# Kernel tuning notes

Measured on AMD Instinct MI355X. Metric: run time of the kernel, lower is better.

Reference implementation:

```python
import jax, jax.numpy as jnp
import numpy as np

B, IN, OUT = 32768, 1024, 1024

def setup_inputs() -> dict:
    key = jax.random.key(0)
    k1, k2, k3 = jax.random.split(key, 3)
    bound = float(np.sqrt(6.0 / (IN + OUT)))  # xavier_uniform gain=1
    x = jax.random.normal(k1, (B, IN), dtype=jnp.float32)
    weight = jax.random.uniform(k2, (OUT, IN), dtype=jnp.float32, minval=-bound, maxval=bound)
    gate = jnp.abs(jax.random.uniform(k3, (OUT, IN), dtype=jnp.float32, minval=-bound, maxval=bound))  # one_sided init
    bias = jnp.zeros((OUT,), dtype=jnp.float32)
    return {"x": x, "weight": weight, "gate": gate, "bias": bias}

def reference(x, weight, gate, bias):
    # in_bin = sign
    layer_in = jnp.sign(x)
    # drop_weights: weight * binarize_gate(gate) where binarize_gate = (sign(gate)+1)/2
    gate_mask = (jnp.sign(gate) + 1.0) * 0.5
    w = weight * gate_mask
    # weight_bin = sign (gated-off entries stay 0 since sign(0)=0)
    w = jnp.sign(w)
    # F.linear: x @ w.T + bias
    layer_out = jnp.einsum('bi,oi->bo', layer_in, w) + bias
    # adaptive scaling: abs-mean of raw input per row, abs-mean of raw weight per output
    in_scale = jnp.mean(jnp.abs(x), axis=1, keepdims=True)       # [B,1]
    weight_scale = jnp.mean(jnp.abs(weight), axis=1)             # [OUT]
    return in_scale * weight_scale * layer_out
```

## Files before the change

### kernel.cpp

```cpp
#include <hip/hip_runtime.h>

#define B_DIM 32768
#define IN_DIM 1024
#define OUT_DIM 1024

typedef int v4i __attribute__((ext_vector_type(4)));
typedef int v16i __attribute__((ext_vector_type(16)));

__device__ __forceinline__ int sgnb(float v) {
    return (v > 0.f) ? 1 : ((v < 0.f) ? 0xff : 0);
}
__device__ __forceinline__ int gsgnb(float w, float g) {
    return (g < 0.f) ? 0 : sgnb(w);
}

__global__ __launch_bounds__(256) void prep_kernel(
    const float* __restrict__ x, const float* __restrict__ w,
    const float* __restrict__ g,
    signed char* __restrict__ sx, signed char* __restrict__ wb,
    float* __restrict__ xscale, float* __restrict__ wscale) {
    const int wave = threadIdx.x >> 6;
    const int lane = threadIdx.x & 63;
    const int bq = blockIdx.x;
    if (bq < B_DIM / 4) {
        const int row = bq * 4 + wave;
        const float4* xr = (const float4*)(x + (size_t)row * IN_DIM);
        int* sr = (int*)(sx + (size_t)row * IN_DIM);
        float asum = 0.f;
#pragma unroll
        for (int it = 0; it < 4; ++it) {
            float4 v = xr[it * 64 + lane];
            asum += fabsf(v.x) + fabsf(v.y) + fabsf(v.z) + fabsf(v.w);
            sr[it * 64 + lane] =
                sgnb(v.x) | (sgnb(v.y) << 8) | (sgnb(v.z) << 16) | (sgnb(v.w) << 24);
        }
#pragma unroll
        for (int off = 32; off >= 1; off >>= 1) asum += __shfl_xor(asum, off, 64);
        if (lane == 0) xscale[row] = asum * (1.0f / IN_DIM);
    } else {
        const int row = (bq - B_DIM / 4) * 4 + wave;
        const float4* wr = (const float4*)(w + (size_t)row * IN_DIM);
        const float4* gr = (const float4*)(g + (size_t)row * IN_DIM);
        int* sr = (int*)(wb + (size_t)row * IN_DIM);
        float asum = 0.f;
#pragma unroll
        for (int it = 0; it < 4; ++it) {
            float4 wv = wr[it * 64 + lane];
            float4 gv = gr[it * 64 + lane];
            asum += fabsf(wv.x) + fabsf(wv.y) + fabsf(wv.z) + fabsf(wv.w);
            sr[it * 64 + lane] = gsgnb(wv.x, gv.x) | (gsgnb(wv.y, gv.y) << 8) |
                                 (gsgnb(wv.z, gv.z) << 16) | (gsgnb(wv.w, gv.w) << 24);
        }
#pragma unroll
        for (int off = 32; off >= 1; off >>= 1) asum += __shfl_xor(asum, off, 64);
        if (lane == 0) wscale[row] = asum * (1.0f / IN_DIM);
    }
}

__global__ __launch_bounds__(512, 2) void gemm_i8_kernel(
    const signed char* __restrict__ A,
    const signed char* __restrict__ Bw,
    const float* __restrict__ xscale,
    const float* __restrict__ wscale,
    const float* __restrict__ bias,
    float* __restrict__ out) {
    __shared__ signed char smA[2][16384];
    __shared__ signed char smB[2][16384];

    const int t = threadIdx.x;
    const int wave = t >> 6, lane = t & 63;
    const int swz = (blockIdx.x & 7) * 64 + (blockIdx.x >> 3);
    const int bm = swz >> 2;
    const int bn = swz & 3;
    const int wr = wave >> 2, wc = wave & 3;
    const int r32 = lane & 31;
    const int kh_eff = ((lane >> 5) << 4) ^ (((lane >> 2) & 1) << 4);

    int aoff[4], boff[2];
#pragma unroll
    for (int m = 0; m < 4; ++m) aoff[m] = (wr * 128 + m * 32 + r32) * 32 + kh_eff;
#pragma unroll
    for (int n = 0; n < 2; ++n) boff[n] = (wc * 64 + n * 32 + r32) * 32 + kh_eff;

    const int soff = wave * 1024 + lane * 16;
    const int s_row = soff >> 5;
    const int s_kh = (soff & 16) ^ (((s_row >> 2) & 1) << 4);
    const size_t arow0 = (size_t)bm * 256;
    const size_t brow0 = (size_t)bn * 256;
    const signed char* aSrc = A + (((size_t)(arow0 + s_row)) << 10) + s_kh;
    const signed char* bSrc = Bw + (((size_t)(brow0 + s_row)) << 10) + s_kh;

    v16i acc[4][2];
#pragma unroll
    for (int m = 0; m < 4; ++m)
#pragma unroll
        for (int n = 0; n < 2; ++n)
#pragma unroll
            for (int j = 0; j < 16; ++j) acc[m][n][j] = 0;

#define ISSUE_A(P, KS, K0)                                                      \
    __builtin_amdgcn_global_load_lds(                                           \
        (const __attribute__((address_space(1))) void*)(aSrc + (K0) + (KS)*32), \
        (__attribute__((address_space(3))) void*)(&smA[P][(KS)*8192] + wave * 1024), \
        16, 0, 0)
#define ISSUE_B(P, KS, K0)                                                      \
    __builtin_amdgcn_global_load_lds(                                           \
        (const __attribute__((address_space(1))) void*)(bSrc + (K0) + (KS)*32), \
        (__attribute__((address_space(3))) void*)(&smB[P][(KS)*8192] + wave * 1024), \
        16, 0, 0)

#define PHASE(P, KS, DOPREF, K0N, VMASM)                                        \
    {                                                                           \
        v4i af[4], bf[2];                                                       \
        _Pragma("unroll") for (int m = 0; m < 4; ++m)                           \
            af[m] = *(const v4i*)(&smA[P][(KS)*8192] + aoff[m]);                \
        _Pragma("unroll") for (int n = 0; n < 2; ++n)                           \
            bf[n] = *(const v4i*)(&smB[P][(KS)*8192] + boff[n]);                \
        if (DOPREF) {                                                           \
            ISSUE_A((P) ^ 1, KS, K0N);                                          \
            ISSUE_B((P) ^ 1, KS, K0N);                                          \
        }                                                                       \
        __builtin_amdgcn_s_barrier();                                           \
        __builtin_amdgcn_s_setprio(1);                                          \
        _Pragma("unroll") for (int m = 0; m < 4; ++m) {                         \
            acc[m][0] = __builtin_amdgcn_mfma_i32_32x32x32_i8(af[m], bf[0],     \
                                                              acc[m][0], 0, 0, 0); \
            acc[m][1] = __builtin_amdgcn_mfma_i32_32x32x32_i8(af[m], bf[1],     \
                                                              acc[m][1], 0, 0, 0); \
        }                                                                       \
        __builtin_amdgcn_s_setprio(0);                                          \
        VMASM;                                                                  \
        __builtin_amdgcn_s_barrier();                                           \
    }

    ISSUE_A(0, 0, 0);
    ISSUE_B(0, 0, 0);
    ISSUE_A(0, 1, 0);
    ISSUE_B(0, 1, 0);
    asm volatile("s_waitcnt vmcnt(2)" ::: "memory");
    __builtin_amdgcn_s_barrier();

#pragma unroll 1
    for (int kt = 0; kt < 14; kt += 2) {
        PHASE(0, 0, 1, (kt + 1) * 64, asm volatile("s_waitcnt vmcnt(2)" ::: "memory"));
        PHASE(0, 1, 1, (kt + 1) * 64, asm volatile("s_waitcnt vmcnt(2)" ::: "memory"));
        PHASE(1, 0, 1, (kt + 2) * 64, asm volatile("s_waitcnt vmcnt(2)" ::: "memory"));
        PHASE(1, 1, 1, (kt + 2) * 64, asm volatile("s_waitcnt vmcnt(2)" ::: "memory"));
    }
    PHASE(0, 0, 1, 15 * 64, asm volatile("s_waitcnt vmcnt(2)" ::: "memory"));
    PHASE(0, 1, 1, 15 * 64, asm volatile("s_waitcnt vmcnt(2)" ::: "memory"));
    PHASE(1, 0, 0, 0, asm volatile("s_waitcnt vmcnt(0)" ::: "memory"));
    PHASE(1, 1, 0, 0, (void)0);

#undef PHASE
#undef ISSUE_A
#undef ISSUE_B

    const int col = lane & 31;
    const int rb = 4 * (lane >> 5);
    float wsc[2], bv[2];
    int gcolv[2];
#pragma unroll
    for (int n = 0; n < 2; ++n) {
        gcolv[n] = bn * 256 + wc * 64 + n * 32 + col;
        wsc[n] = wscale[gcolv[n]];
        bv[n] = bias[gcolv[n]];
    }
#pragma unroll
    for (int m = 0; m < 4; ++m) {
#pragma unroll
        for (int j = 0; j < 16; ++j) {
            const int grow = bm * 256 + wr * 128 + m * 32 + (j & 3) + 8 * (j >> 2) + rb;
            const float is = xscale[grow];
#pragma unroll
            for (int n = 0; n < 2; ++n) {
                out[(size_t)grow * OUT_DIM + gcolv[n]] =
                    is * wsc[n] * ((float)acc[m][n][j] + bv[n]);
            }
        }
    }
}

extern "C" void kernel_launch(void* const* d_in, const int* in_sizes, int n_in,
                              void* d_out, int out_size, void* d_ws, size_t ws_size,
                              hipStream_t stream) {
    const float* x = (const float*)d_in[0];
    const float* w = (const float*)d_in[1];
    const float* g = (const float*)d_in[2];
    const float* bias = (const float*)d_in[3];
    float* out = (float*)d_out;

    signed char* sx = (signed char*)d_ws;
    signed char* wb = sx + (size_t)B_DIM * IN_DIM;
    float* xscale = (float*)(wb + (size_t)OUT_DIM * IN_DIM);
    float* wscale = xscale + B_DIM;

    prep_kernel<<<B_DIM / 4 + OUT_DIM / 4, 256, 0, stream>>>(x, w, g, sx, wb,
                                                             xscale, wscale);
    gemm_i8_kernel<<<(B_DIM / 256) * (OUT_DIM / 256), 512, 0, stream>>>(
        sx, wb, xscale, wscale, bias, out);
}
```

Measured before the change: 288.3 us.

## Deepen int8 GEMM LDS pipeline to four stages with 64-byte K tiles

```diff
diff --git a/kernel.cpp b/kernel.cpp
--- a/kernel.cpp
+++ b/kernel.cpp
@@ -64,8 +64,8 @@
     const float* __restrict__ wscale,
     const float* __restrict__ bias,
     float* __restrict__ out) {
-    __shared__ signed char smA[2][16384];
-    __shared__ signed char smB[2][16384];
+    __shared__ signed char smA[4][16384];
+    __shared__ signed char smB[4][16384];
 
     const int t = threadIdx.x;
     const int wave = t >> 6, lane = t & 63;
@@ -74,21 +74,20 @@
     const int bn = swz & 3;
     const int wr = wave >> 2, wc = wave & 3;
     const int r32 = lane & 31;
-    const int kh_eff = ((lane >> 5) << 4) ^ (((lane >> 2) & 1) << 4);
+    const int kh = (lane >> 5) << 4;
+    const int fsw = ((r32 >> 1) & 3) << 4;
+    const int c0 = kh ^ fsw;
 
     int aoff[4], boff[2];
 #pragma unroll
-    for (int m = 0; m < 4; ++m) aoff[m] = (wr * 128 + m * 32 + r32) * 32 + kh_eff;
-#pragma unroll
-    for (int n = 0; n < 2; ++n) boff[n] = (wc * 64 + n * 32 + r32) * 32 + kh_eff;
-
-    const int soff = wave * 1024 + lane * 16;
-    const int s_row = soff >> 5;
-    const int s_kh = (soff & 16) ^ (((s_row >> 2) & 1) << 4);
-    const size_t arow0 = (size_t)bm * 256;
-    const size_t brow0 = (size_t)bn * 256;
-    const signed char* aSrc = A + (((size_t)(arow0 + s_row)) << 10) + s_kh;
-    const signed char* bSrc = Bw + (((size_t)(brow0 + s_row)) << 10) + s_kh;
+    for (int m = 0; m < 4; ++m) aoff[m] = (wr * 128 + m * 32 + r32) * 64 + c0;
+#pragma unroll
+    for (int n = 0; n < 2; ++n) boff[n] = (wc * 64 + n * 32 + r32) * 64 + c0;
+
+    const int sc = (((t & 3) ^ ((t >> 3) & 3)) << 4);
+    const signed char* aS = A + ((size_t)(bm * 256 + (t >> 2)) << 10) + sc;
+    const signed char* bS = Bw + ((size_t)(bn * 256 + (t >> 2)) << 10) + sc;
+    const int ldsW = wave * 1024;
 
     v16i acc[4][2];
 #pragma unroll
@@ -98,28 +97,29 @@
 #pragma unroll
             for (int j = 0; j < 16; ++j) acc[m][n][j] = 0;
 
-#define ISSUE_A(P, KS, K0)                                                      \
+#define GLDS(SRC, DST)                                                          \
     __builtin_amdgcn_global_load_lds(                                           \
-        (const __attribute__((address_space(1))) void*)(aSrc + (K0) + (KS)*32), \
-        (__attribute__((address_space(3))) void*)(&smA[P][(KS)*8192] + wave * 1024), \
-        16, 0, 0)
-#define ISSUE_B(P, KS, K0)                                                      \
-    __builtin_amdgcn_global_load_lds(                                           \
-        (const __attribute__((address_space(1))) void*)(bSrc + (K0) + (KS)*32), \
-        (__attribute__((address_space(3))) void*)(&smB[P][(KS)*8192] + wave * 1024), \
-        16, 0, 0)
-
-#define PHASE(P, KS, DOPREF, K0N, VMASM)                                        \
+        (const __attribute__((address_space(1))) void*)(SRC),                   \
+        (__attribute__((address_space(3))) void*)(DST), 16, 0, 0)
+#define ISSUE_A(NB, KT)                                                         \
+    do {                                                                        \
+        GLDS(aS + (KT)*64, &smA[NB][ldsW]);                                     \
+        GLDS(aS + 131072 + (KT)*64, &smA[NB][8192 + ldsW]);                     \
+    } while (0)
+#define ISSUE_B(NB, KT)                                                         \
+    do {                                                                        \
+        GLDS(bS + (KT)*64, &smB[NB][ldsW]);                                     \
+        GLDS(bS + 131072 + (KT)*64, &smB[NB][8192 + ldsW]);                     \
+    } while (0)
+
+#define PHASE(BUF, KS, ISSUES, WAITS)                                           \
     {                                                                           \
         v4i af[4], bf[2];                                                       \
         _Pragma("unroll") for (int m = 0; m < 4; ++m)                           \
-            af[m] = *(const v4i*)(&smA[P][(KS)*8192] + aoff[m]);                \
+            af[m] = *(const v4i*)(&smA[BUF][aoff[m] ^ ((KS) << 5)]);            \
         _Pragma("unroll") for (int n = 0; n < 2; ++n)                           \
-            bf[n] = *(const v4i*)(&smB[P][(KS)*8192] + boff[n]);                \
-        if (DOPREF) {                                                           \
-            ISSUE_A((P) ^ 1, KS, K0N);                                          \
-            ISSUE_B((P) ^ 1, KS, K0N);                                          \
-        }                                                                       \
+            bf[n] = *(const v4i*)(&smB[BUF][boff[n] ^ ((KS) << 5)]);            \
+        ISSUES;                                                                 \
         __builtin_amdgcn_s_barrier();                                           \
         __builtin_amdgcn_s_setprio(1);                                          \
         _Pragma("unroll") for (int m = 0; m < 4; ++m) {                         \
@@ -129,32 +129,38 @@
                                                               acc[m][1], 0, 0, 0); \
         }                                                                       \
         __builtin_amdgcn_s_setprio(0);                                          \
-        VMASM;                                                                  \
+        WAITS;                                                                  \
         __builtin_amdgcn_s_barrier();                                           \
     }
 
-    ISSUE_A(0, 0, 0);
-    ISSUE_B(0, 0, 0);
-    ISSUE_A(0, 1, 0);
-    ISSUE_B(0, 1, 0);
-    asm volatile("s_waitcnt vmcnt(2)" ::: "memory");
+    ISSUE_A(0, 0);
+    ISSUE_B(0, 0);
+    ISSUE_A(1, 1);
+    ISSUE_B(1, 1);
+    ISSUE_A(2, 2);
+    ISSUE_B(2, 2);
+    asm volatile("s_waitcnt vmcnt(8)" ::: "memory");
     __builtin_amdgcn_s_barrier();
 
 #pragma unroll 1
-    for (int kt = 0; kt < 14; kt += 2) {
-        PHASE(0, 0, 1, (kt + 1) * 64, asm volatile("s_waitcnt vmcnt(2)" ::: "memory"));
-        PHASE(0, 1, 1, (kt + 1) * 64, asm volatile("s_waitcnt vmcnt(2)" ::: "memory"));
-        PHASE(1, 0, 1, (kt + 2) * 64, asm volatile("s_waitcnt vmcnt(2)" ::: "memory"));
-        PHASE(1, 1, 1, (kt + 2) * 64, asm volatile("s_waitcnt vmcnt(2)" ::: "memory"));
-    }
-    PHASE(0, 0, 1, 15 * 64, asm volatile("s_waitcnt vmcnt(2)" ::: "memory"));
-    PHASE(0, 1, 1, 15 * 64, asm volatile("s_waitcnt vmcnt(2)" ::: "memory"));
-    PHASE(1, 0, 0, 0, asm volatile("s_waitcnt vmcnt(0)" ::: "memory"));
-    PHASE(1, 1, 0, 0, (void)0);
+    for (int j = 0; j < 13; ++j) {
+        const int buf = j & 3;
+        const int nbuf = (j + 3) & 3;
+        const int kn = (j + 3) * 64;
+        PHASE(buf, 0, ISSUE_A(nbuf, kn / 64 * 64 / 64), (void)0);
+        PHASE(buf, 1, ISSUE_B(nbuf, kn / 64 * 64 / 64), asm volatile("s_waitcnt vmcnt(8)" ::: "memory"));
+    }
+    PHASE(1, 0, (void)0, (void)0);
+    PHASE(1, 1, (void)0, asm volatile("s_waitcnt vmcnt(4)" ::: "memory"));
+    PHASE(2, 0, (void)0, (void)0);
+    PHASE(2, 1, (void)0, asm volatile("s_waitcnt vmcnt(0)" ::: "memory"));
+    PHASE(3, 0, (void)0, (void)0);
+    PHASE(3, 1, (void)0, (void)0);
 
 #undef PHASE
 #undef ISSUE_A
 #undef ISSUE_B
+#undef GLDS
 
     const int col = lane & 31;
     const int rb = 4 * (lane >> 5);
```

New measurement: 283.7 us. Within noise of the previous version (-1.6%).
